# Kernel tuning notes

Hardware: AMD Instinct MI355X
Metric: run time of the kernel (lower is better)

## Reference

```python
import jax, jax.numpy as jnp
import numpy as np
import math

C, N, D, D_CTX = 256, 512, 256, 256
K = 24
HOMEOSTASIS = 0.01
FEEDBACK = 0.3
B = 64


def setup_inputs() -> dict:
    key = jax.random.key(0)
    k1, k2, k3, k4, k5 = jax.random.split(key, 5)
    ff_scale = math.sqrt(2.0 / (D + N))
    ctx_scale = math.sqrt(2.0 / (D_CTX + N))
    pred_scale = math.sqrt(2.0 / (N + D))
    return {
        "x_input": jax.random.normal(k1, (B, D), dtype=jnp.float32),
        "x_context": jax.random.normal(k2, (B, D_CTX), dtype=jnp.float32),
        "W_ff": jax.random.normal(k3, (C, D, N), dtype=jnp.float32) * ff_scale,
        "W_ctx": jax.random.normal(k4, (C, D_CTX, N), dtype=jnp.float32) * ctx_scale,
        "W_pred": jax.random.normal(k5, (C, N, D), dtype=jnp.float32) * pred_scale,
        "bias": jnp.zeros((C, N), dtype=jnp.float32),
        "avg_activity": jnp.full((C, N), 0.05, dtype=jnp.float32),
    }


def _k_winners(drive, avg_activity, k):
    # homeostatic boosting: boost * homeostasis * 100
    boost = jnp.log1p(0.05 / (avg_activity + 1e-6))  # [C, N]
    boosted = drive + boost[None] * (HOMEOSTASIS * 100.0)
    topk_vals = jax.lax.top_k(boosted, k)[0]  # [B, C, k]
    threshold = jax.lax.stop_gradient(topk_vals[..., -1:])  # [B, C, 1]
    mask = (boosted >= threshold).astype(drive.dtype)
    activation = jax.nn.relu(drive) * mask
    activation = activation / (jnp.sum(activation, axis=-1, keepdims=True) + 1e-8) * k
    return activation


def reference(x_input, x_context, W_ff, W_ctx, W_pred, bias, avg_activity):
    # per-column feedforward + context drive: [B, C, N]
    ff_drive = jnp.einsum('bd,cdn->bcn', x_input, W_ff)
    ctx_drive = jnp.einsum('bd,cdn->bcn', x_context, W_ctx)
    drive = ff_drive + ctx_drive * FEEDBACK + bias[None]
    activations = _k_winners(drive, avg_activity, K)  # [B, C, N]
    predictions = jnp.einsum('bcn,cnd->bcd', activations, W_pred)  # [B, C, D]
    errors = x_input[:, None, :] - predictions  # [B, C, D]
    return activations, predictions, errors
```

## Files before the change

kernel.cpp:

```cpp
#include <hip/hip_runtime.h>
#include <math.h>

#define CC 256
#define NN 512
#define DD 256
#define BB 64
#define KK 24
#define WCAP 48

__global__ void transpose_x_kernel(const float* __restrict__ x_in,
                                   const float* __restrict__ x_ctx,
                                   float* __restrict__ xT) {
  int idx = blockIdx.x * blockDim.x + threadIdx.x;
  int d = idx >> 6;
  int b = idx & 63;
  float v = (d < DD) ? x_in[b * DD + d] : 0.3f * x_ctx[b * DD + (d - DD)];
  xT[idx] = v;
}

__launch_bounds__(512)
__global__ void drive_gemm(const float* __restrict__ xT,
                           const float* __restrict__ W_ff,
                           const float* __restrict__ W_ctx,
                           const float* __restrict__ bias,
                           const float* __restrict__ avg_act,
                           float* __restrict__ driveB) {
  const int c = blockIdx.x >> 1;
  const int nh = blockIdx.x & 1;
  const int t = threadIdx.x;
  const int ng = t & 127;
  const int n0 = nh * 256 + ng * 2;
  const int b0 = __builtin_amdgcn_readfirstlane((t >> 7) * 16);

  float2 acc[16];
#pragma unroll
  for (int i = 0; i < 16; ++i) { acc[i].x = 0.f; acc[i].y = 0.f; }

  for (int m = 0; m < 2; ++m) {
    const float* __restrict__ wp =
        (m == 0 ? W_ff : W_ctx) + (size_t)c * DD * NN + n0;
    const float* __restrict__ xbase = xT + (m * DD) * BB + b0;

    float2 bufA[4], bufB[4];
#pragma unroll
    for (int j = 0; j < 4; ++j)
      bufA[j] = *reinterpret_cast<const float2*>(wp + (size_t)j * NN);

#pragma unroll 1
    for (int d = 0; d < DD; d += 8) {
#pragma unroll
      for (int j = 0; j < 4; ++j) {
        int dn = d + 4 + j;
        dn = (dn < DD) ? dn : (DD - 1);
        bufB[j] = *reinterpret_cast<const float2*>(wp + (size_t)dn * NN);
      }
#pragma unroll
      for (int j = 0; j < 4; ++j) {
        const float* __restrict__ xp = xbase + (d + j) * BB;
        const float2 w = bufA[j];
#pragma unroll
        for (int i = 0; i < 16; ++i) {
          acc[i].x = fmaf(xp[i], w.x, acc[i].x);
          acc[i].y = fmaf(xp[i], w.y, acc[i].y);
        }
      }
#pragma unroll
      for (int j = 0; j < 4; ++j) {
        int dn = d + 8 + j;
        dn = (dn < DD) ? dn : (DD - 1);
        bufA[j] = *reinterpret_cast<const float2*>(wp + (size_t)dn * NN);
      }
#pragma unroll
      for (int j = 0; j < 4; ++j) {
        const float* __restrict__ xp = xbase + (d + 4 + j) * BB;
        const float2 w = bufB[j];
#pragma unroll
        for (int i = 0; i < 16; ++i) {
          acc[i].x = fmaf(xp[i], w.x, acc[i].x);
          acc[i].y = fmaf(xp[i], w.y, acc[i].y);
        }
      }
    }
  }

  const float2 bz = *reinterpret_cast<const float2*>(bias + (size_t)c * NN + n0);
  const float2 av = *reinterpret_cast<const float2*>(avg_act + (size_t)c * NN + n0);
  float2 bo;
  bo.x = log1pf(0.05f / (av.x + 1e-6f));
  bo.y = log1pf(0.05f / (av.y + 1e-6f));

#pragma unroll
  for (int i = 0; i < 16; ++i) {
    float2 m2;
    m2.x = (acc[i].x + bz.x) + bo.x;
    m2.y = (acc[i].y + bz.y) + bo.y;
    *reinterpret_cast<float2*>(driveB + ((size_t)c * BB + (b0 + i)) * NN + n0) = m2;
  }
}

__launch_bounds__(512)
__global__ void sparse_pred(const float* __restrict__ x_in,
                            const float* __restrict__ driveB,
                            const float* __restrict__ W_pred,
                            const float* __restrict__ avg_act,
                            float* __restrict__ out_act,
                            float* __restrict__ out_pred,
                            float* __restrict__ out_err) {
  __shared__ int wcnt[32];
  __shared__ float wlist[32 * WCAP * 2];

  const int c = blockIdx.x >> 1;
  const int bh = blockIdx.x & 1;
  const int t = threadIdx.x;
  const int lane = t & 63;
  const int wv = t >> 6;

  float bo[8];
#pragma unroll
  for (int j = 0; j < 8; ++j)
    bo[j] = log1pf(0.05f / (avg_act[(size_t)c * NN + lane + 64 * j] + 1e-6f));

  for (int r = wv * 4; r < wv * 4 + 4; ++r) {
    const int b = bh * 32 + r;
    const float* __restrict__ row = driveB + ((size_t)c * BB + b) * NN;
    float o[8], v[8];
#pragma unroll
    for (int j = 0; j < 8; ++j) { o[j] = row[lane + 64 * j]; v[j] = o[j]; }

    float kth = 0.f;
    for (int it = 0; it < KK; ++it) {
      float m = v[0];
#pragma unroll
      for (int j = 1; j < 8; ++j) m = fmaxf(m, v[j]);
#pragma unroll
      for (int off = 1; off <= 32; off <<= 1) m = fmaxf(m, __shfl_xor(m, off));
      kth = m;
      bool mine = false;
#pragma unroll
      for (int j = 0; j < 8; ++j) mine = mine || (v[j] == m);
      unsigned long long msk = __ballot(mine);
      int first = __ffsll(msk) - 1;
      if (lane == first) {
        bool done = false;
#pragma unroll
        for (int j = 0; j < 8; ++j) {
          bool cnd = (!done) && (v[j] == m);
          if (cnd) v[j] = -INFINITY;
          done = done || cnd;
        }
      }
    }

    float raw[8];
    float s = 0.f;
#pragma unroll
    for (int j = 0; j < 8; ++j) {
      const float rw = (o[j] >= kth) ? fmaxf(o[j] - bo[j], 0.f) : 0.f;
      raw[j] = rw;
      s += rw;
    }
#pragma unroll
    for (int off = 1; off <= 32; off <<= 1) s += __shfl_xor(s, off);
    const float sc = (float)KK / (s + 1e-8f);

    int base = 0;
#pragma unroll
    for (int j = 0; j < 8; ++j) {
      const int n = lane + 64 * j;
      const float a = raw[j] * sc;
      out_act[(size_t)b * (CC * NN) + (size_t)c * NN + n] = a;
      const bool win = a > 0.f;
      unsigned long long m = __ballot(win);
      int pos = base + __popcll(m & ((1ull << lane) - 1ull));
      if (win && pos < WCAP) {
        const int slot = (r * WCAP + pos) * 2;
        wlist[slot] = a;
        reinterpret_cast<int*>(wlist)[slot + 1] = n;
      }
      base += (int)__popcll(m);
    }
    if (lane == 0) wcnt[r] = (base < WCAP) ? base : WCAP;
  }
  __syncthreads();

  {
    const int dq = t & 63;
    const int d0 = dq * 4;
    const int grp = t >> 6;
    const float* __restrict__ wp = W_pred + (size_t)c * NN * DD;
    for (int bi = 0; bi < 4; ++bi) {
      const int r = grp * 4 + bi;
      const int b = bh * 32 + r;
      const int cnt = wcnt[r];
      float4 p0 = make_float4(0.f, 0.f, 0.f, 0.f);
      float4 p1 = make_float4(0.f, 0.f, 0.f, 0.f);
      float4 p2 = make_float4(0.f, 0.f, 0.f, 0.f);
      float4 p3 = make_float4(0.f, 0.f, 0.f, 0.f);
      int i = 0;
      for (; i + 4 <= cnt; i += 4) {
        const int s0 = (r * WCAP + i) * 2;
        const float a0 = wlist[s0 + 0];
        const int n0 = reinterpret_cast<const int*>(wlist)[s0 + 1];
        const float a1 = wlist[s0 + 2];
        const int n1 = reinterpret_cast<const int*>(wlist)[s0 + 3];
        const float a2 = wlist[s0 + 4];
        const int n2 = reinterpret_cast<const int*>(wlist)[s0 + 5];
        const float a3 = wlist[s0 + 6];
        const int n3 = reinterpret_cast<const int*>(wlist)[s0 + 7];
        const float4 w0 = *reinterpret_cast<const float4*>(wp + (size_t)n0 * DD + d0);
        const float4 w1 = *reinterpret_cast<const float4*>(wp + (size_t)n1 * DD + d0);
        const float4 w2 = *reinterpret_cast<const float4*>(wp + (size_t)n2 * DD + d0);
        const float4 w3 = *reinterpret_cast<const float4*>(wp + (size_t)n3 * DD + d0);
        p0.x = fmaf(a0, w0.x, p0.x); p0.y = fmaf(a0, w0.y, p0.y);
        p0.z = fmaf(a0, w0.z, p0.z); p0.w = fmaf(a0, w0.w, p0.w);
        p1.x = fmaf(a1, w1.x, p1.x); p1.y = fmaf(a1, w1.y, p1.y);
        p1.z = fmaf(a1, w1.z, p1.z); p1.w = fmaf(a1, w1.w, p1.w);
        p2.x = fmaf(a2, w2.x, p2.x); p2.y = fmaf(a2, w2.y, p2.y);
        p2.z = fmaf(a2, w2.z, p2.z); p2.w = fmaf(a2, w2.w, p2.w);
        p3.x = fmaf(a3, w3.x, p3.x); p3.y = fmaf(a3, w3.y, p3.y);
        p3.z = fmaf(a3, w3.z, p3.z); p3.w = fmaf(a3, w3.w, p3.w);
      }
      for (; i < cnt; ++i) {
        const int s0 = (r * WCAP + i) * 2;
        const float a0 = wlist[s0];
        const int n0 = reinterpret_cast<const int*>(wlist)[s0 + 1];
        const float4 w0 = *reinterpret_cast<const float4*>(wp + (size_t)n0 * DD + d0);
        p0.x = fmaf(a0, w0.x, p0.x); p0.y = fmaf(a0, w0.y, p0.y);
        p0.z = fmaf(a0, w0.z, p0.z); p0.w = fmaf(a0, w0.w, p0.w);
      }
      float4 r4;
      r4.x = (p0.x + p1.x) + (p2.x + p3.x);
      r4.y = (p0.y + p1.y) + (p2.y + p3.y);
      r4.z = (p0.z + p1.z) + (p2.z + p3.z);
      r4.w = (p0.w + p1.w) + (p2.w + p3.w);
      const float4 xi = *reinterpret_cast<const float4*>(x_in + (size_t)b * DD + d0);
      float4 e4;
      e4.x = xi.x - r4.x; e4.y = xi.y - r4.y; e4.z = xi.z - r4.z; e4.w = xi.w - r4.w;
      *reinterpret_cast<float4*>(out_pred + (size_t)b * (CC * DD) + (size_t)c * DD + d0) = r4;
      *reinterpret_cast<float4*>(out_err + (size_t)b * (CC * DD) + (size_t)c * DD + d0) = e4;
    }
  }
}

#define MAT_F (BB * NN)
#define FSMEM_FLOATS (MAT_F + BB + BB + NN + BB + BB * WCAP * 2)
#define FSMEM_BYTES (FSMEM_FLOATS * 4)

__launch_bounds__(1024)
__global__ void cortical_fused(const float* __restrict__ x_in,
                               const float* __restrict__ xT,
                               const float* __restrict__ W_ff,
                               const float* __restrict__ W_ctx,
                               const float* __restrict__ W_pred,
                               const float* __restrict__ bias,
                               const float* __restrict__ avg_act,
                               float* __restrict__ out_act,
                               float* __restrict__ out_pred,
                               float* __restrict__ out_err) {
  extern __shared__ float smem[];
  float* mat = smem;
  float* thr = smem + MAT_F;
  float* scl = thr + BB;
  float* boostS = scl + BB;
  int* wcnt = (int*)(boostS + NN);
  float* wlist = (float*)(wcnt + BB);

  const int c = blockIdx.x;
  const int t = threadIdx.x;
  const int lane = t & 63;
  const int wv = t >> 6;

  if (t < NN) boostS[t] = log1pf(0.05f / (avg_act[c * NN + t] + 1e-6f));
  __syncthreads();

  const int ng = t & 255;
  const int n0 = ng * 2;
  const int b0 = __builtin_amdgcn_readfirstlane((t >> 8) * 16);

  float acc[16][2];
#pragma unroll
  for (int i = 0; i < 16; ++i) { acc[i][0] = 0.f; acc[i][1] = 0.f; }

  const float* __restrict__ wf = W_ff + (size_t)c * DD * NN + n0;
  const float* __restrict__ wc = W_ctx + (size_t)c * DD * NN + n0;

#pragma unroll 4
  for (int d = 0; d < DD; ++d) {
    const float2 w = *reinterpret_cast<const float2*>(wf + (size_t)d * NN);
    const float* __restrict__ xp = xT + d * BB + b0;
#pragma unroll
    for (int i = 0; i < 16; ++i) {
      const float xv = xp[i];
      acc[i][0] = fmaf(xv, w.x, acc[i][0]);
      acc[i][1] = fmaf(xv, w.y, acc[i][1]);
    }
  }
#pragma unroll 4
  for (int d = 0; d < DD; ++d) {
    const float2 w = *reinterpret_cast<const float2*>(wc + (size_t)d * NN);
    const float* __restrict__ xp = xT + (DD + d) * BB + b0;
#pragma unroll
    for (int i = 0; i < 16; ++i) {
      const float xv = xp[i];
      acc[i][0] = fmaf(xv, w.x, acc[i][0]);
      acc[i][1] = fmaf(xv, w.y, acc[i][1]);
    }
  }

  const float2 bz = *reinterpret_cast<const float2*>(bias + (size_t)c * NN + n0);
  const float2 bo = *reinterpret_cast<const float2*>(boostS + n0);
#pragma unroll
  for (int i = 0; i < 16; ++i) {
    float2 m2;
    m2.x = (acc[i][0] + bz.x) + bo.x;
    m2.y = (acc[i][1] + bz.y) + bo.y;
    *reinterpret_cast<float2*>(mat + (size_t)(b0 + i) * NN + n0) = m2;
  }
  __syncthreads();

  for (int r = wv * 4; r < wv * 4 + 4; ++r) {
    float v[8];
#pragma unroll
    for (int j = 0; j < 8; ++j) v[j] = mat[r * NN + lane + 64 * j];
    float kth = 0.f;
    for (int it = 0; it < KK; ++it) {
      float m = v[0];
#pragma unroll
      for (int j = 1; j < 8; ++j) m = fmaxf(m, v[j]);
#pragma unroll
      for (int off = 1; off <= 32; off <<= 1) m = fmaxf(m, __shfl_xor(m, off));
      kth = m;
      bool mine = false;
#pragma unroll
      for (int j = 0; j < 8; ++j) mine = mine || (v[j] == m);
      unsigned long long msk = __ballot(mine);
      int first = __ffsll(msk) - 1;
      if (lane == first) {
        bool done = false;
#pragma unroll
        for (int j = 0; j < 8; ++j) {
          bool cnd = (!done) && (v[j] == m);
          if (cnd) v[j] = -INFINITY;
          done = done || cnd;
        }
      }
    }
    if (lane == 0) thr[r] = kth;
  }
  __syncthreads();

  for (int r = wv * 4; r < wv * 4 + 4; ++r) {
    const float tb = thr[r];
    float raw[8];
    float s = 0.f;
#pragma unroll
    for (int j = 0; j < 8; ++j) {
      const int n = lane + 64 * j;
      const float bv = mat[r * NN + n];
      const float rw = (bv >= tb) ? fmaxf(bv - boostS[n], 0.f) : 0.f;
      raw[j] = rw;
      s += rw;
    }
#pragma unroll
    for (int off = 1; off <= 32; off <<= 1) s += __shfl_xor(s, off);
    const float sc = (float)KK / (s + 1e-8f);

    int base = 0;
#pragma unroll
    for (int j = 0; j < 8; ++j) {
      const int n = lane + 64 * j;
      const float a = raw[j] * sc;
      out_act[(size_t)r * (CC * NN) + (size_t)c * NN + n] = a;
      const bool win = a > 0.f;
      unsigned long long m = __ballot(win);
      int pos = base + __popcll(m & ((1ull << lane) - 1ull));
      if (win && pos < WCAP) {
        const int slot = (r * WCAP + pos) * 2;
        wlist[slot] = a;
        reinterpret_cast<int*>(wlist)[slot + 1] = n;
      }
      base += (int)__popcll(m);
    }
    if (lane == 0) wcnt[r] = (base < WCAP) ? base : WCAP;
  }
  __syncthreads();

  {
    const int dq = t & 63;
    const int d0 = dq * 4;
    const int grp = t >> 6;
    const float* __restrict__ wp = W_pred + (size_t)c * NN * DD;
    for (int bi = 0; bi < 4; ++bi) {
      const int b = grp * 4 + bi;
      const int cnt = wcnt[b];
      float4 p = make_float4(0.f, 0.f, 0.f, 0.f);
      float4 q = make_float4(0.f, 0.f, 0.f, 0.f);
      int i = 0;
      for (; i + 2 <= cnt; i += 2) {
        const int s0 = (b * WCAP + i) * 2;
        const int s1 = s0 + 2;
        const float a0 = wlist[s0];
        const int nn0 = reinterpret_cast<const int*>(wlist)[s0 + 1];
        const float a1 = wlist[s1];
        const int nn1 = reinterpret_cast<const int*>(wlist)[s1 + 1];
        const float4 w0 = *reinterpret_cast<const float4*>(wp + (size_t)nn0 * DD + d0);
        const float4 w1 = *reinterpret_cast<const float4*>(wp + (size_t)nn1 * DD + d0);
        p.x = fmaf(a0, w0.x, p.x); p.y = fmaf(a0, w0.y, p.y);
        p.z = fmaf(a0, w0.z, p.z); p.w = fmaf(a0, w0.w, p.w);
        q.x = fmaf(a1, w1.x, q.x); q.y = fmaf(a1, w1.y, q.y);
        q.z = fmaf(a1, w1.z, q.z); q.w = fmaf(a1, w1.w, q.w);
      }
      if (i < cnt) {
        const int s0 = (b * WCAP + i) * 2;
        const float a0 = wlist[s0];
        const int nn0 = reinterpret_cast<const int*>(wlist)[s0 + 1];
        const float4 w0 = *reinterpret_cast<const float4*>(wp + (size_t)nn0 * DD + d0);
        p.x = fmaf(a0, w0.x, p.x); p.y = fmaf(a0, w0.y, p.y);
        p.z = fmaf(a0, w0.z, p.z); p.w = fmaf(a0, w0.w, p.w);
      }
      float4 r4;
      r4.x = p.x + q.x; r4.y = p.y + q.y; r4.z = p.z + q.z; r4.w = p.w + q.w;
      const float4 xi = *reinterpret_cast<const float4*>(x_in + (size_t)b * DD + d0);
      float4 e4;
      e4.x = xi.x - r4.x; e4.y = xi.y - r4.y; e4.z = xi.z - r4.z; e4.w = xi.w - r4.w;
      *reinterpret_cast<float4*>(out_pred + (size_t)b * (CC * DD) + (size_t)c * DD + d0) = r4;
      *reinterpret_cast<float4*>(out_err + (size_t)b * (CC * DD) + (size_t)c * DD + d0) = e4;
    }
  }
}

extern "C" void kernel_launch(void* const* d_in, const int* in_sizes, int n_in,
                              void* d_out, int out_size, void* d_ws, size_t ws_size,
                              hipStream_t stream) {
  const float* x_in = (const float*)d_in[0];
  const float* x_ctx = (const float*)d_in[1];
  const float* W_ff = (const float*)d_in[2];
  const float* W_ctx = (const float*)d_in[3];
  const float* W_pred = (const float*)d_in[4];
  const float* bias = (const float*)d_in[5];
  const float* avg = (const float*)d_in[6];

  float* out = (float*)d_out;
  float* out_act = out;
  float* out_pred = out + (size_t)BB * CC * NN;
  float* out_err = out_pred + (size_t)BB * CC * DD;

  float* xT = (float*)d_ws;
  float* driveB = xT + 2 * BB * DD;

  const size_t need_bytes = (size_t)(2 * BB * DD + (size_t)CC * BB * NN) * 4;

  transpose_x_kernel<<<(2 * BB * DD) / 256, 256, 0, stream>>>(x_in, x_ctx, xT);

  if (ws_size >= need_bytes) {
    drive_gemm<<<2 * CC, 512, 0, stream>>>(xT, W_ff, W_ctx, bias, avg, driveB);
    sparse_pred<<<2 * CC, 512, 0, stream>>>(x_in, driveB, W_pred, avg, out_act,
                                            out_pred, out_err);
  } else {
    hipFuncSetAttribute((const void*)cortical_fused,
                        hipFuncAttributeMaxDynamicSharedMemorySize, FSMEM_BYTES);
    cortical_fused<<<CC, 1024, FSMEM_BYTES, stream>>>(x_in, xT, W_ff, W_ctx,
                                                      W_pred, bias, avg, out_act,
                                                      out_pred, out_err);
  }
}
```

Baseline: 243.7 us.

## Split drive GEMM reduction dimension across two thread halves with LDS reduction

The drive GEMM now uses 1024 threads per block, with each half of the block accumulating over half of the D dimension for both W_ff and W_ctx. Partial sums are combined through a 64KB shared-memory buffer before the bias and boost are added. The manual double-buffered weight prefetch is replaced by a simple unroll-4 loop. The aim is more waves in flight to hide weight-load latency, at the cost of a sync, extra LDS traffic and tighter register limits from the launch bounds.

Result: faster. 231.2 us (-5.1%).

```diff
diff --git a/kernel.cpp b/kernel.cpp
--- a/kernel.cpp
+++ b/kernel.cpp
@@ -7,6 +7,8 @@
 #define BB 64
 #define KK 24
 #define WCAP 48
+
+#define RED_BYTES (32 * 512 * 4)
 
 __global__ void transpose_x_kernel(const float* __restrict__ x_in,
                                    const float* __restrict__ x_ctx,
@@ -18,83 +20,79 @@
   xT[idx] = v;
 }
 
-__launch_bounds__(512)
+__launch_bounds__(1024, 8)
 __global__ void drive_gemm(const float* __restrict__ xT,
                            const float* __restrict__ W_ff,
                            const float* __restrict__ W_ctx,
                            const float* __restrict__ bias,
                            const float* __restrict__ avg_act,
                            float* __restrict__ driveB) {
+  extern __shared__ float red[];
+
   const int c = blockIdx.x >> 1;
   const int nh = blockIdx.x & 1;
   const int t = threadIdx.x;
-  const int ng = t & 127;
+  const int half = t >> 9;
+  const int tt = t & 511;
+  const int ng = tt & 127;
   const int n0 = nh * 256 + ng * 2;
-  const int b0 = __builtin_amdgcn_readfirstlane((t >> 7) * 16);
+  const int b0 = __builtin_amdgcn_readfirstlane((tt >> 7) * 16);
+  const int d0 = __builtin_amdgcn_readfirstlane((t >> 9) * 128);
 
   float2 acc[16];
 #pragma unroll
   for (int i = 0; i < 16; ++i) { acc[i].x = 0.f; acc[i].y = 0.f; }
 
-  for (int m = 0; m < 2; ++m) {
-    const float* __restrict__ wp =
-        (m == 0 ? W_ff : W_ctx) + (size_t)c * DD * NN + n0;
-    const float* __restrict__ xbase = xT + (m * DD) * BB + b0;
-
-    float2 bufA[4], bufB[4];
-#pragma unroll
-    for (int j = 0; j < 4; ++j)
-      bufA[j] = *reinterpret_cast<const float2*>(wp + (size_t)j * NN);
-
-#pragma unroll 1
-    for (int d = 0; d < DD; d += 8) {
-#pragma unroll
-      for (int j = 0; j < 4; ++j) {
-        int dn = d + 4 + j;
-        dn = (dn < DD) ? dn : (DD - 1);
-        bufB[j] = *reinterpret_cast<const float2*>(wp + (size_t)dn * NN);
-      }
-#pragma unroll
-      for (int j = 0; j < 4; ++j) {
-        const float* __restrict__ xp = xbase + (d + j) * BB;
-        const float2 w = bufA[j];
-#pragma unroll
-        for (int i = 0; i < 16; ++i) {
-          acc[i].x = fmaf(xp[i], w.x, acc[i].x);
-          acc[i].y = fmaf(xp[i], w.y, acc[i].y);
-        }
-      }
-#pragma unroll
-      for (int j = 0; j < 4; ++j) {
-        int dn = d + 8 + j;
-        dn = (dn < DD) ? dn : (DD - 1);
-        bufA[j] = *reinterpret_cast<const float2*>(wp + (size_t)dn * NN);
-      }
-#pragma unroll
-      for (int j = 0; j < 4; ++j) {
-        const float* __restrict__ xp = xbase + (d + 4 + j) * BB;
-        const float2 w = bufB[j];
-#pragma unroll
-        for (int i = 0; i < 16; ++i) {
-          acc[i].x = fmaf(xp[i], w.x, acc[i].x);
-          acc[i].y = fmaf(xp[i], w.y, acc[i].y);
-        }
-      }
-    }
-  }
-
-  const float2 bz = *reinterpret_cast<const float2*>(bias + (size_t)c * NN + n0);
-  const float2 av = *reinterpret_cast<const float2*>(avg_act + (size_t)c * NN + n0);
-  float2 bo;
-  bo.x = log1pf(0.05f / (av.x + 1e-6f));
-  bo.y = log1pf(0.05f / (av.y + 1e-6f));
-
-#pragma unroll
-  for (int i = 0; i < 16; ++i) {
-    float2 m2;
-    m2.x = (acc[i].x + bz.x) + bo.x;
-    m2.y = (acc[i].y + bz.y) + bo.y;
-    *reinterpret_cast<float2*>(driveB + ((size_t)c * BB + (b0 + i)) * NN + n0) = m2;
+  {
+    const float* __restrict__ wp = W_ff + (size_t)c * DD * NN + (size_t)d0 * NN + n0;
+    const float* __restrict__ xbase = xT + d0 * BB + b0;
+#pragma unroll 4
+    for (int d = 0; d < 128; ++d) {
+      const float2 w = *reinterpret_cast<const float2*>(wp + (size_t)d * NN);
+      const float* __restrict__ xp = xbase + d * BB;
+#pragma unroll
+      for (int i = 0; i < 16; ++i) {
+        acc[i].x = fmaf(xp[i], w.x, acc[i].x);
+        acc[i].y = fmaf(xp[i], w.y, acc[i].y);
+      }
+    }
+  }
+  {
+    const float* __restrict__ wp = W_ctx + (size_t)c * DD * NN + (size_t)d0 * NN + n0;
+    const float* __restrict__ xbase = xT + (DD + d0) * BB + b0;
+#pragma unroll 4
+    for (int d = 0; d < 128; ++d) {
+      const float2 w = *reinterpret_cast<const float2*>(wp + (size_t)d * NN);
+      const float* __restrict__ xp = xbase + d * BB;
+#pragma unroll
+      for (int i = 0; i < 16; ++i) {
+        acc[i].x = fmaf(xp[i], w.x, acc[i].x);
+        acc[i].y = fmaf(xp[i], w.y, acc[i].y);
+      }
+    }
+  }
+
+  if (half == 0) {
+#pragma unroll
+    for (int i = 0; i < 16; ++i) {
+      red[(2 * i) * 512 + tt] = acc[i].x;
+      red[(2 * i + 1) * 512 + tt] = acc[i].y;
+    }
+  }
+  __syncthreads();
+  if (half == 1) {
+    const float2 bz = *reinterpret_cast<const float2*>(bias + (size_t)c * NN + n0);
+    const float2 av = *reinterpret_cast<const float2*>(avg_act + (size_t)c * NN + n0);
+    float2 bo;
+    bo.x = log1pf(0.05f / (av.x + 1e-6f));
+    bo.y = log1pf(0.05f / (av.y + 1e-6f));
+#pragma unroll
+    for (int i = 0; i < 16; ++i) {
+      float2 m2;
+      m2.x = (acc[i].x + red[(2 * i) * 512 + tt]) + bz.x + bo.x;
+      m2.y = (acc[i].y + red[(2 * i + 1) * 512 + tt]) + bz.y + bo.y;
+      *reinterpret_cast<float2*>(driveB + ((size_t)c * BB + (b0 + i)) * NN + n0) = m2;
+    }
   }
 }
 
@@ -453,7 +451,10 @@
   transpose_x_kernel<<<(2 * BB * DD) / 256, 256, 0, stream>>>(x_in, x_ctx, xT);
 
   if (ws_size >= need_bytes) {
-    drive_gemm<<<2 * CC, 512, 0, stream>>>(xT, W_ff, W_ctx, bias, avg, driveB);
+    hipFuncSetAttribute((const void*)drive_gemm,
+                        hipFuncAttributeMaxDynamicSharedMemorySize, RED_BYTES);
+    drive_gemm<<<2 * CC, 1024, RED_BYTES, stream>>>(xT, W_ff, W_ctx, bias, avg,
+                                                    driveB);
     sparse_pred<<<2 * CC, 512, 0, stream>>>(x_in, driveB, W_pred, avg, out_act,
                                             out_pred, out_err);
   } else {
```

## Stage x operand in LDS and use one 1024-thread block per column in drive GEMM

Applied to the files above, without the earlier changes.

The drive GEMM now copies the whole transposed x (ff and scaled ctx, 128 KB) into shared memory once per block and reads it with float4 broadcasts instead of scalar global loads. Each block covers one full column with 1024 threads rather than splitting it across two 512-thread blocks, and the weight prefetch depth grows from 4 to 8 rows. This is meant to cut redundant global/L2 traffic for x and raise memory-level parallelism on the weight stream. The cost is 128 KB of LDS per block, which limits occupancy to one block per CU, adds a staging phase before any compute, and leaves only 256 blocks.

Measured after the change: 259.1 us. +6.3%, slower.

```diff
diff --git a/kernel.cpp b/kernel.cpp
--- a/kernel.cpp
+++ b/kernel.cpp
@@ -7,6 +7,8 @@
 #define BB 64
 #define KK 24
 #define WCAP 48
+
+#define XSMEM_BYTES (2 * DD * BB * 4)
 
 __global__ void transpose_x_kernel(const float* __restrict__ x_in,
                                    const float* __restrict__ x_ctx,
@@ -18,68 +20,82 @@
   xT[idx] = v;
 }
 
-__launch_bounds__(512)
+#define FMA16(W, XPTR)                                                        \
+  do {                                                                        \
+    const float4* __restrict__ xp = reinterpret_cast<const float4*>(XPTR);    \
+    const float4 x0 = xp[0], x1 = xp[1], x2 = xp[2], x3 = xp[3];              \
+    acc[0].x = fmaf(x0.x, (W).x, acc[0].x);   acc[0].y = fmaf(x0.x, (W).y, acc[0].y);   \
+    acc[1].x = fmaf(x0.y, (W).x, acc[1].x);   acc[1].y = fmaf(x0.y, (W).y, acc[1].y);   \
+    acc[2].x = fmaf(x0.z, (W).x, acc[2].x);   acc[2].y = fmaf(x0.z, (W).y, acc[2].y);   \
+    acc[3].x = fmaf(x0.w, (W).x, acc[3].x);   acc[3].y = fmaf(x0.w, (W).y, acc[3].y);   \
+    acc[4].x = fmaf(x1.x, (W).x, acc[4].x);   acc[4].y = fmaf(x1.x, (W).y, acc[4].y);   \
+    acc[5].x = fmaf(x1.y, (W).x, acc[5].x);   acc[5].y = fmaf(x1.y, (W).y, acc[5].y);   \
+    acc[6].x = fmaf(x1.z, (W).x, acc[6].x);   acc[6].y = fmaf(x1.z, (W).y, acc[6].y);   \
+    acc[7].x = fmaf(x1.w, (W).x, acc[7].x);   acc[7].y = fmaf(x1.w, (W).y, acc[7].y);   \
+    acc[8].x = fmaf(x2.x, (W).x, acc[8].x);   acc[8].y = fmaf(x2.x, (W).y, acc[8].y);   \
+    acc[9].x = fmaf(x2.y, (W).x, acc[9].x);   acc[9].y = fmaf(x2.y, (W).y, acc[9].y);   \
+    acc[10].x = fmaf(x2.z, (W).x, acc[10].x); acc[10].y = fmaf(x2.z, (W).y, acc[10].y); \
+    acc[11].x = fmaf(x2.w, (W).x, acc[11].x); acc[11].y = fmaf(x2.w, (W).y, acc[11].y); \
+    acc[12].x = fmaf(x3.x, (W).x, acc[12].x); acc[12].y = fmaf(x3.x, (W).y, acc[12].y); \
+    acc[13].x = fmaf(x3.y, (W).x, acc[13].x); acc[13].y = fmaf(x3.y, (W).y, acc[13].y); \
+    acc[14].x = fmaf(x3.z, (W).x, acc[14].x); acc[14].y = fmaf(x3.z, (W).y, acc[14].y); \
+    acc[15].x = fmaf(x3.w, (W).x, acc[15].x); acc[15].y = fmaf(x3.w, (W).y, acc[15].y); \
+  } while (0)
+
+__launch_bounds__(1024)
 __global__ void drive_gemm(const float* __restrict__ xT,
                            const float* __restrict__ W_ff,
                            const float* __restrict__ W_ctx,
                            const float* __restrict__ bias,
                            const float* __restrict__ avg_act,
                            float* __restrict__ driveB) {
-  const int c = blockIdx.x >> 1;
-  const int nh = blockIdx.x & 1;
+  extern __shared__ float xs[];
+
+  const int c = blockIdx.x;
   const int t = threadIdx.x;
-  const int ng = t & 127;
-  const int n0 = nh * 256 + ng * 2;
-  const int b0 = __builtin_amdgcn_readfirstlane((t >> 7) * 16);
+
+  {
+    const float4* __restrict__ src = reinterpret_cast<const float4*>(xT);
+    float4* dst = reinterpret_cast<float4*>(xs);
+#pragma unroll
+    for (int i = 0; i < 8; ++i) dst[t + 1024 * i] = src[t + 1024 * i];
+  }
+  __syncthreads();
+
+  const int n0 = (t & 255) * 2;
+  const int b0 = __builtin_amdgcn_readfirstlane((t >> 8) * 16);
 
   float2 acc[16];
 #pragma unroll
   for (int i = 0; i < 16; ++i) { acc[i].x = 0.f; acc[i].y = 0.f; }
 
+#pragma unroll 1
   for (int m = 0; m < 2; ++m) {
     const float* __restrict__ wp =
         (m == 0 ? W_ff : W_ctx) + (size_t)c * DD * NN + n0;
-    const float* __restrict__ xbase = xT + (m * DD) * BB + b0;
-
-    float2 bufA[4], bufB[4];
-#pragma unroll
-    for (int j = 0; j < 4; ++j)
-      bufA[j] = *reinterpret_cast<const float2*>(wp + (size_t)j * NN);
+    const float* __restrict__ xb = xs + m * (DD * BB) + b0;
+
+    float2 wa[8], wb[8];
+#pragma unroll
+    for (int j = 0; j < 8; ++j)
+      wa[j] = *reinterpret_cast<const float2*>(wp + (size_t)j * NN);
 
 #pragma unroll 1
-    for (int d = 0; d < DD; d += 8) {
-#pragma unroll
-      for (int j = 0; j < 4; ++j) {
-        int dn = d + 4 + j;
-        dn = (dn < DD) ? dn : (DD - 1);
-        bufB[j] = *reinterpret_cast<const float2*>(wp + (size_t)dn * NN);
-      }
-#pragma unroll
-      for (int j = 0; j < 4; ++j) {
-        const float* __restrict__ xp = xbase + (d + j) * BB;
-        const float2 w = bufA[j];
-#pragma unroll
-        for (int i = 0; i < 16; ++i) {
-          acc[i].x = fmaf(xp[i], w.x, acc[i].x);
-          acc[i].y = fmaf(xp[i], w.y, acc[i].y);
-        }
-      }
-#pragma unroll
-      for (int j = 0; j < 4; ++j) {
-        int dn = d + 8 + j;
-        dn = (dn < DD) ? dn : (DD - 1);
-        bufA[j] = *reinterpret_cast<const float2*>(wp + (size_t)dn * NN);
-      }
-#pragma unroll
-      for (int j = 0; j < 4; ++j) {
-        const float* __restrict__ xp = xbase + (d + 4 + j) * BB;
-        const float2 w = bufB[j];
-#pragma unroll
-        for (int i = 0; i < 16; ++i) {
-          acc[i].x = fmaf(xp[i], w.x, acc[i].x);
-          acc[i].y = fmaf(xp[i], w.y, acc[i].y);
-        }
-      }
+    for (int d0 = 0; d0 < DD; d0 += 16) {
+#pragma unroll
+      for (int j = 0; j < 8; ++j) {
+        const int dn = (d0 + 8 + j) & 255;
+        wb[j] = *reinterpret_cast<const float2*>(wp + (size_t)dn * NN);
+      }
+#pragma unroll
+      for (int j = 0; j < 8; ++j) FMA16(wa[j], xb + (d0 + j) * BB);
+#pragma unroll
+      for (int j = 0; j < 8; ++j) {
+        const int dn = (d0 + 16 + j) & 255;
+        wa[j] = *reinterpret_cast<const float2*>(wp + (size_t)dn * NN);
+      }
+#pragma unroll
+      for (int j = 0; j < 8; ++j) FMA16(wb[j], xb + (d0 + 8 + j) * BB);
     }
   }
 
@@ -453,7 +469,10 @@
   transpose_x_kernel<<<(2 * BB * DD) / 256, 256, 0, stream>>>(x_in, x_ctx, xT);
 
   if (ws_size >= need_bytes) {
-    drive_gemm<<<2 * CC, 512, 0, stream>>>(xT, W_ff, W_ctx, bias, avg, driveB);
+    hipFuncSetAttribute((const void*)drive_gemm,
+                        hipFuncAttributeMaxDynamicSharedMemorySize, XSMEM_BYTES);
+    drive_gemm<<<CC, 1024, XSMEM_BYTES, stream>>>(xT, W_ff, W_ctx, bias, avg,
+                                                  driveB);
     sparse_pred<<<2 * CC, 512, 0, stream>>>(x_in, driveB, W_pred, avg, out_act,
                                             out_pred, out_err);
   } else {
```
